# Performance work log

Hardware: AMD Instinct MI355X
Metric: run time of the kernel (lower is better)

The kernel has to match this reference:

```python
import jax, jax.numpy as jnp
import numpy as np

B, V, M, C = 1024, 2, 256, 256  # batch, num_vars (must be 2), latent states, categories


def setup_inputs() -> dict:
    key = jax.random.key(0)
    k1, k2, k3 = jax.random.split(key, 3)
    x = jax.random.randint(k1, (B, V), 0, C)
    # input-node tables: per var v, per latent node k, a [M, C] row-normalized table
    W = jax.nn.softmax(jax.random.normal(k2, (V, M, M, C), dtype=jnp.float32), axis=-1)
    # sum-node mixture weights over the M product children
    w_sum = jax.nn.softmax(jax.random.normal(k3, (M,), dtype=jnp.float32))
    return {"x": x, "W": W, "w_sum": w_sum}


def reference(x, W, w_sum):
    # lp[v] has shape [M(k), M(m), B]: log W[v, k, m, x[b, v]]
    # (matches torch: probs[:, x_var].log() per input node, stacked over latent k)
    lp0 = jnp.log(W[0][:, :, x[:, 0]])  # [M, M, B]
    lp1 = jnp.log(W[1][:, :, x[:, 1]])  # [M, M, B]
    prod = lp0 + lp1                    # product nodes, [M(k), M, B]
    # sum node: log( sum_k w_k * exp(prod_k) ) -> [M, B]
    mixed = jnp.log(jnp.einsum('k,kmb->mb', w_sum, jnp.exp(prod)))
    # root: logsumexp over the leading M dim -> [B]
    return jax.nn.logsumexp(mixed, axis=0)
```

## Files before the change

### kernel.cpp

```cpp
#include <hip/hip_runtime.h>
#include <math.h>


#define SPLITS  128
#define KCHUNK  512
#define BK      32
#define NITER   (KCHUNK / BK)
#define LDSS    40

typedef float  f32x4  __attribute__((ext_vector_type(4)));
typedef short  bf16x8 __attribute__((ext_vector_type(8)));

static __device__ __forceinline__ short f2bf(float f) {
    unsigned u = __builtin_bit_cast(unsigned, f);
    u += 0x7fffu + ((u >> 16) & 1u);
    return (short)(u >> 16);
}

template <bool USE_PART>
__global__ __launch_bounds__(512, 2) void gemm_s_kernel(
    const float* __restrict__ W, const float* __restrict__ wsum,
    float* __restrict__ out_acc)
{
    __shared__ short As[256 * LDSS];
    __shared__ short Bs[128 * LDSS];

    const int  c1tile = blockIdx.x;
    const int  split  = blockIdx.y;
    const long kbase  = (long)split * KCHUNK;

    const float* __restrict__ Ag = W;
    const float* __restrict__ Bg = W + 16777216 + (long)c1tile * 128;

    const int t = threadIdx.x;
    const int cqA = (t & 63) * 4;
    const int kqA = (t >> 6) * 4;
    const int cqB = (t & 31) * 4;
    const int kqB = (t >> 5) * 2;

    const int lane = t & 63;
    const int wv   = t >> 6;
    const int wc0  = (wv & 3) * 64;
    const int wc1  = (wv >> 2) * 64;
    const int ml   = lane & 15;
    const int qd   = lane >> 4;

    const float w0 = wsum[split * 2];
    const float w1 = wsum[split * 2 + 1];

    f32x4 acc[4][4];
#pragma unroll
    for (int i = 0; i < 4; ++i)
#pragma unroll
        for (int j = 0; j < 4; ++j) acc[i][j] = (f32x4){0.f, 0.f, 0.f, 0.f};

    for (int it = 0; it < NITER; ++it) {
        const long  k0 = kbase + (long)it * BK;
        const float wk = (it < NITER / 2) ? w0 : w1;
        float4 a4[4], b4[2];
#pragma unroll
        for (int r = 0; r < 4; ++r)
            a4[r] = *(const float4*)(Ag + (k0 + kqA + r) * 256 + cqA);
#pragma unroll
        for (int r = 0; r < 2; ++r)
            b4[r] = *(const float4*)(Bg + (k0 + kqB + r) * 256 + cqB);
        __syncthreads();
        const float* af32 = reinterpret_cast<const float*>(a4);
        const float* bf32 = reinterpret_cast<const float*>(b4);
#pragma unroll
        for (int j = 0; j < 4; ++j) {
            short4 av;
            av.x = f2bf(af32[0 * 4 + j] * wk);
            av.y = f2bf(af32[1 * 4 + j] * wk);
            av.z = f2bf(af32[2 * 4 + j] * wk);
            av.w = f2bf(af32[3 * 4 + j] * wk);
            *(short4*)&As[(cqA + j) * LDSS + kqA] = av;
            short2 bv;
            bv.x = f2bf(bf32[0 * 4 + j]);
            bv.y = f2bf(bf32[1 * 4 + j]);
            *(short2*)&Bs[(cqB + j) * LDSS + kqB] = bv;
        }
        __syncthreads();
        bf16x8 afr[4];
#pragma unroll
        for (int mi = 0; mi < 4; ++mi)
            afr[mi] = *(const bf16x8*)&As[(wc0 + mi * 16 + ml) * LDSS + qd * 8];
#pragma unroll
        for (int ni = 0; ni < 4; ++ni) {
            const bf16x8 bfr = *(const bf16x8*)&Bs[(wc1 + ni * 16 + ml) * LDSS + qd * 8];
#pragma unroll
            for (int mi = 0; mi < 4; ++mi)
                acc[mi][ni] = __builtin_amdgcn_mfma_f32_16x16x32_bf16(
                    afr[mi], bfr, acc[mi][ni], 0, 0, 0);
        }
    }

    if (USE_PART) {
        float* __restrict__ Pb = out_acc + ((size_t)split * 2 + c1tile) * 32768;
#pragma unroll
        for (int mi = 0; mi < 4; ++mi) {
            const int row0 = wc0 + mi * 16 + qd * 4;
#pragma unroll
            for (int ni = 0; ni < 4; ++ni) {
                const int col = wc1 + ni * 16 + ml;
#pragma unroll
                for (int r = 0; r < 4; ++r)
                    Pb[(row0 + r) * 128 + col] = acc[mi][ni][r];
            }
        }
    } else {
#pragma unroll
        for (int mi = 0; mi < 4; ++mi) {
            const int row0 = wc0 + mi * 16 + qd * 4;
#pragma unroll
            for (int ni = 0; ni < 4; ++ni) {
                const int col = c1tile * 128 + wc1 + ni * 16 + ml;
#pragma unroll
                for (int r = 0; r < 4; ++r)
                    atomicAdd(&out_acc[(row0 + r) * 256 + col], acc[mi][ni][r]);
            }
        }
    }
}

__global__ __launch_bounds__(64) void finish_part_kernel(
    const int* __restrict__ x, const float* __restrict__ P, float* __restrict__ out)
{
    const int b  = blockIdx.x;
    const int t  = threadIdx.x;
    const int x0 = x[2 * b], x1 = x[2 * b + 1];
    const int t1 = x1 >> 7;
    const size_t base = (size_t)x0 * 128 + (x1 & 127);
    float v = P[((size_t)t * 2 + t1) * 32768 + base]
            + P[((size_t)(t + 64) * 2 + t1) * 32768 + base];
#pragma unroll
    for (int off = 32; off > 0; off >>= 1) v += __shfl_down(v, off);
    if (t == 0) out[b] = logf(v);
}

__global__ __launch_bounds__(64) void finish_atom_kernel(
    const int* __restrict__ x, const float* __restrict__ S, float* __restrict__ out)
{
    const int b  = blockIdx.x * 64 + threadIdx.x;
    const int x0 = x[2 * b], x1 = x[2 * b + 1];
    out[b] = logf(S[x0 * 256 + x1]);
}

extern "C" void kernel_launch(void* const* d_in, const int* in_sizes, int n_in,
                              void* d_out, int out_size, void* d_ws, size_t ws_size,
                              hipStream_t stream)
{
    const int*   x    = (const int*)d_in[0];
    const float* W    = (const float*)d_in[1];
    const float* wsum = (const float*)d_in[2];
    float* out = (float*)d_out;

    const size_t part_bytes = (size_t)SPLITS * 2 * 32768 * sizeof(float);

    if (ws_size >= part_bytes) {
        float* P = (float*)d_ws;
        gemm_s_kernel<true><<<dim3(2, SPLITS), 512, 0, stream>>>(W, wsum, P);
        finish_part_kernel<<<dim3(1024), 64, 0, stream>>>(x, P, out);
    } else {
        float* S = (float*)d_ws;
        hipMemsetAsync(d_ws, 0, 65536 * sizeof(float), stream);
        gemm_s_kernel<false><<<dim3(2, SPLITS), 512, 0, stream>>>(W, wsum, S);
        finish_atom_kernel<<<dim3(16), 64, 0, stream>>>(x, S, out);
    }
}
```

Before: 209.9 us.

## Fuse per-latent GEMM with x-gather, one block per latent state

Each block now computes the full 256x256 product tile for one latent k (K=256 over m), instead of splitting across two column tiles and combining two k's per split. Inside the block it stages the accumulator through shared memory in four 64-row passes and gathers only the entries indexed by x, writing a weighted [B,256] buffer. A small finish kernel then reduces over k and takes the log. This removes the large partial-sum buffer write and readback (about 32 MB) and drops the atomic fallback. In exchange it uses 64 KB of dynamic shared memory, a larger accumulator per thread (128 floats), and now relies on the workspace being large enough for G.

Result: faster. 201.2 us (-4.2%).

```diff
diff --git a/kernel.cpp b/kernel.cpp
--- a/kernel.cpp
+++ b/kernel.cpp
@@ -2,11 +2,10 @@
 #include <math.h>
 
 
-#define SPLITS  128
-#define KCHUNK  512
-#define BK      32
-#define NITER   (KCHUNK / BK)
-#define LDSS    40
+#define KCHUNK 256
+#define BK     32
+#define NITER  (KCHUNK / BK)
+#define LDSS   40
 
 typedef float  f32x4  __attribute__((ext_vector_type(4)));
 typedef short  bf16x8 __attribute__((ext_vector_type(8)));
@@ -17,68 +16,60 @@
     return (short)(u >> 16);
 }
 
-template <bool USE_PART>
-__global__ __launch_bounds__(512, 2) void gemm_s_kernel(
-    const float* __restrict__ W, const float* __restrict__ wsum,
-    float* __restrict__ out_acc)
+__global__ __launch_bounds__(512, 2) void gemm_gather_kernel(
+    const int* __restrict__ x, const float* __restrict__ W,
+    const float* __restrict__ wsum, float* __restrict__ G)
 {
-    __shared__ short As[256 * LDSS];
-    __shared__ short Bs[128 * LDSS];
+    extern __shared__ char smem[];
+    short* __restrict__ As = (short*)smem;
+    short* __restrict__ Bs = (short*)(smem + 256 * LDSS * 2);
+    float* __restrict__ Sg = (float*)smem;
 
-    const int  c1tile = blockIdx.x;
-    const int  split  = blockIdx.y;
-    const long kbase  = (long)split * KCHUNK;
+    const int  split = blockIdx.x;
+    const long kbase = (long)split * KCHUNK;
+    const float* __restrict__ Ag = W + kbase * 256;
+    const float* __restrict__ Bg = W + 16777216 + kbase * 256;
 
-    const float* __restrict__ Ag = W;
-    const float* __restrict__ Bg = W + 16777216 + (long)c1tile * 128;
-
-    const int t = threadIdx.x;
-    const int cqA = (t & 63) * 4;
-    const int kqA = (t >> 6) * 4;
-    const int cqB = (t & 31) * 4;
-    const int kqB = (t >> 5) * 2;
+    const int t  = threadIdx.x;
+    const int cq = (t & 63) * 4;
+    const int kq = (t >> 6) * 4;
 
     const int lane = t & 63;
     const int wv   = t >> 6;
     const int wc0  = (wv & 3) * 64;
-    const int wc1  = (wv >> 2) * 64;
+    const int wc1  = (wv >> 2) * 128;
     const int ml   = lane & 15;
     const int qd   = lane >> 4;
 
-    const float w0 = wsum[split * 2];
-    const float w1 = wsum[split * 2 + 1];
-
-    f32x4 acc[4][4];
+    f32x4 acc[4][8];
 #pragma unroll
     for (int i = 0; i < 4; ++i)
 #pragma unroll
-        for (int j = 0; j < 4; ++j) acc[i][j] = (f32x4){0.f, 0.f, 0.f, 0.f};
+        for (int j = 0; j < 8; ++j) acc[i][j] = (f32x4){0.f, 0.f, 0.f, 0.f};
 
     for (int it = 0; it < NITER; ++it) {
-        const long  k0 = kbase + (long)it * BK;
-        const float wk = (it < NITER / 2) ? w0 : w1;
-        float4 a4[4], b4[2];
+        float4 a4[4], b4[4];
 #pragma unroll
-        for (int r = 0; r < 4; ++r)
-            a4[r] = *(const float4*)(Ag + (k0 + kqA + r) * 256 + cqA);
-#pragma unroll
-        for (int r = 0; r < 2; ++r)
-            b4[r] = *(const float4*)(Bg + (k0 + kqB + r) * 256 + cqB);
+        for (int r = 0; r < 4; ++r) {
+            a4[r] = *(const float4*)(Ag + (long)(it * BK + kq + r) * 256 + cq);
+            b4[r] = *(const float4*)(Bg + (long)(it * BK + kq + r) * 256 + cq);
+        }
         __syncthreads();
-        const float* af32 = reinterpret_cast<const float*>(a4);
-        const float* bf32 = reinterpret_cast<const float*>(b4);
+        const float* af = reinterpret_cast<const float*>(a4);
+        const float* bf = reinterpret_cast<const float*>(b4);
 #pragma unroll
         for (int j = 0; j < 4; ++j) {
-            short4 av;
-            av.x = f2bf(af32[0 * 4 + j] * wk);
-            av.y = f2bf(af32[1 * 4 + j] * wk);
-            av.z = f2bf(af32[2 * 4 + j] * wk);
-            av.w = f2bf(af32[3 * 4 + j] * wk);
-            *(short4*)&As[(cqA + j) * LDSS + kqA] = av;
-            short2 bv;
-            bv.x = f2bf(bf32[0 * 4 + j]);
-            bv.y = f2bf(bf32[1 * 4 + j]);
-            *(short2*)&Bs[(cqB + j) * LDSS + kqB] = bv;
+            short4 av, bv;
+            av.x = f2bf(af[0 * 4 + j]);
+            av.y = f2bf(af[1 * 4 + j]);
+            av.z = f2bf(af[2 * 4 + j]);
+            av.w = f2bf(af[3 * 4 + j]);
+            *(short4*)&As[(cq + j) * LDSS + kq] = av;
+            bv.x = f2bf(bf[0 * 4 + j]);
+            bv.y = f2bf(bf[1 * 4 + j]);
+            bv.z = f2bf(bf[2 * 4 + j]);
+            bv.w = f2bf(bf[3 * 4 + j]);
+            *(short4*)&Bs[(cq + j) * LDSS + kq] = bv;
         }
         __syncthreads();
         bf16x8 afr[4];
@@ -86,7 +77,7 @@
         for (int mi = 0; mi < 4; ++mi)
             afr[mi] = *(const bf16x8*)&As[(wc0 + mi * 16 + ml) * LDSS + qd * 8];
 #pragma unroll
-        for (int ni = 0; ni < 4; ++ni) {
+        for (int ni = 0; ni < 8; ++ni) {
             const bf16x8 bfr = *(const bf16x8*)&Bs[(wc1 + ni * 16 + ml) * LDSS + qd * 8];
 #pragma unroll
             for (int mi = 0; mi < 4; ++mi)
@@ -95,55 +86,42 @@
         }
     }
 
-    if (USE_PART) {
-        float* __restrict__ Pb = out_acc + ((size_t)split * 2 + c1tile) * 32768;
+    const int b0 = t, b1 = t + 512;
+    const int2 xa = ((const int2*)x)[b0];
+    const int2 xb = ((const int2*)x)[b1];
+    float v0 = 0.f, v1 = 0.f;
 #pragma unroll
-        for (int mi = 0; mi < 4; ++mi) {
-            const int row0 = wc0 + mi * 16 + qd * 4;
+    for (int q = 0; q < 4; ++q) {
+        __syncthreads();
+        if (wc0 == q * 64) {
 #pragma unroll
-            for (int ni = 0; ni < 4; ++ni) {
-                const int col = wc1 + ni * 16 + ml;
+            for (int mi = 0; mi < 4; ++mi)
 #pragma unroll
-                for (int r = 0; r < 4; ++r)
-                    Pb[(row0 + r) * 128 + col] = acc[mi][ni][r];
-            }
+                for (int ni = 0; ni < 8; ++ni)
+#pragma unroll
+                    for (int r = 0; r < 4; ++r)
+                        Sg[(mi * 16 + qd * 4 + r) * 256 + wc1 + ni * 16 + ml] =
+                            acc[mi][ni][r];
         }
-    } else {
-#pragma unroll
-        for (int mi = 0; mi < 4; ++mi) {
-            const int row0 = wc0 + mi * 16 + qd * 4;
-#pragma unroll
-            for (int ni = 0; ni < 4; ++ni) {
-                const int col = c1tile * 128 + wc1 + ni * 16 + ml;
-#pragma unroll
-                for (int r = 0; r < 4; ++r)
-                    atomicAdd(&out_acc[(row0 + r) * 256 + col], acc[mi][ni][r]);
-            }
-        }
+        __syncthreads();
+        if ((xa.x >> 6) == q) v0 = Sg[(xa.x & 63) * 256 + xa.y];
+        if ((xb.x >> 6) == q) v1 = Sg[(xb.x & 63) * 256 + xb.y];
     }
+    const float w = wsum[split];
+    G[(long)b0 * 256 + split] = v0 * w;
+    G[(long)b1 * 256 + split] = v1 * w;
 }
 
-__global__ __launch_bounds__(64) void finish_part_kernel(
-    const int* __restrict__ x, const float* __restrict__ P, float* __restrict__ out)
+__global__ __launch_bounds__(256) void finish_kernel(
+    const float* __restrict__ G, float* __restrict__ out)
 {
-    const int b  = blockIdx.x;
-    const int t  = threadIdx.x;
-    const int x0 = x[2 * b], x1 = x[2 * b + 1];
-    const int t1 = x1 >> 7;
-    const size_t base = (size_t)x0 * 128 + (x1 & 127);
-    float v = P[((size_t)t * 2 + t1) * 32768 + base]
-            + P[((size_t)(t + 64) * 2 + t1) * 32768 + base];
+    const int b    = blockIdx.x * 4 + (threadIdx.x >> 6);
+    const int lane = threadIdx.x & 63;
+    const float4 g = ((const float4*)(G + (long)b * 256))[lane];
+    float v = (g.x + g.y) + (g.z + g.w);
 #pragma unroll
     for (int off = 32; off > 0; off >>= 1) v += __shfl_down(v, off);
-    if (t == 0) out[b] = logf(v);
-}
-
-__global__ __launch_bounds__(64) void finish_atom_kernel(
-    const int* __restrict__ x, const float* __restrict__ S, float* __restrict__ out)
-{
-    const int b  = blockIdx.x * 64 + threadIdx.x;
-    const int x0 = x[2 * b], x1 = x[2 * b + 1];
-    out[b] = logf(S[x0 * 256 + x1]);
+    if (lane == 0) out[b] = logf(v);
 }
 
 extern "C" void kernel_launch(void* const* d_in, const int* in_sizes, int n_in,
@@ -153,18 +131,9 @@
     const int*   x    = (const int*)d_in[0];
     const float* W    = (const float*)d_in[1];
     const float* wsum = (const float*)d_in[2];
+    float* G   = (float*)d_ws;
     float* out = (float*)d_out;
 
-    const size_t part_bytes = (size_t)SPLITS * 2 * 32768 * sizeof(float);
-
-    if (ws_size >= part_bytes) {
-        float* P = (float*)d_ws;
-        gemm_s_kernel<true><<<dim3(2, SPLITS), 512, 0, stream>>>(W, wsum, P);
-        finish_part_kernel<<<dim3(1024), 64, 0, stream>>>(x, P, out);
-    } else {
-        float* S = (float*)d_ws;
-        hipMemsetAsync(d_ws, 0, 65536 * sizeof(float), stream);
-        gemm_s_kernel<false><<<dim3(2, SPLITS), 512, 0, stream>>>(W, wsum, S);
-        finish_atom_kernel<<<dim3(16), 64, 0, stream>>>(x, S, out);
-    }
+    gemm_gather_kernel<<<dim3(256), 512, 65536, stream>>>(x, W, wsum, G);
+    finish_kernel<<<dim3(256), 256, 0, stream>>>(G, out);
 }
```
